# Performance work log

Measured on AMD Instinct MI355X. Metric: run time of the kernel, lower is better.

Reference implementation:

```python
import jax, jax.numpy as jnp
import numpy as np

B, C_IN, S = 2, 512, 1024
D, H, HD = 768, 12, 64
E, K, L = 8, 2, 2
FF = 2048
NFFT, HOP, WIN = 1024, 256, 1024
PAD = (WIN - HOP) // 2
FBINS = NFFT // 2 + 1


def _rope(x):
    # interleaved-pair RoPE over the full hidden dim (module builds RoPE with dim=hidden_dim)
    b, s, d = x.shape
    half = d // 2
    inv = 1.0 / (10000.0 ** (jnp.arange(half, dtype=jnp.float32) / half))
    ang = jnp.arange(s, dtype=jnp.float32)[:, None] * inv[None, :]  # [S, half]
    cos, sin = jnp.cos(ang), jnp.sin(ang)
    xr = x.reshape(b, s, half, 2)
    x1, x2 = xr[..., 0], xr[..., 1]
    return jnp.stack([x1 * cos - x2 * sin, x1 * sin + x2 * cos], -1).reshape(b, s, d)


def _ln(x, g, b):
    m = x.mean(-1, keepdims=True)
    v = ((x - m) ** 2).mean(-1, keepdims=True)
    return (x - m) * jax.lax.rsqrt(v + 1e-5) * g + b


def _attn(x, wq, bq, wk, bk, wv, bv, wo, bo, use_rope):
    b, s, d = x.shape
    q, k, v = x @ wq + bq, x @ wk + bk, x @ wv + bv
    if use_rope:
        q, k = _rope(q), _rope(k)
    q = q.reshape(b, s, H, HD).transpose(0, 2, 1, 3)
    k = k.reshape(b, s, H, HD).transpose(0, 2, 1, 3)
    v = v.reshape(b, s, H, HD).transpose(0, 2, 1, 3)
    scores = jnp.einsum('bhqd,bhkd->bhqk', q, k) * (1.0 / np.sqrt(HD))
    causal = jnp.tril(jnp.ones((s, s), bool))
    scores = jnp.where(causal, scores, jnp.float32(-1e30))
    att = jax.nn.softmax(scores, -1)
    out = jnp.einsum('bhqk,bhkd->bhqd', att, v).transpose(0, 2, 1, 3).reshape(b, s, d)
    return out @ wo + bo


def _moe(x, gw, w1, b1, w2, b2):
    # top-k softmax gating, 2-layer GELU experts, sparse combine
    logits = x @ gw  # [B,S,E]
    topv, topi = jax.lax.top_k(logits, K)
    wts = jax.nn.softmax(topv, -1)  # [B,S,K]
    gate = (wts[..., None] * jax.nn.one_hot(topi, E, dtype=x.dtype)).sum(2)  # [B,S,E]
    h = jax.nn.gelu(jnp.einsum('bsd,edf->bsef', x, w1) + b1)
    y = jnp.einsum('bsef,efd->bsed', h, w2) + b2  # [B,S,E,D]
    return jnp.einsum('bse,bsed->bsd', gate, y)


def _istft_same(spec):
    # Vocos-style 'same' ISTFT: irfft -> window -> overlap-add -> normalize -> trim pad
    b, f, t = spec.shape
    n = jnp.arange(WIN, dtype=jnp.float32)
    win = 0.5 * (1.0 - jnp.cos(2.0 * jnp.pi * n / WIN))  # periodic hann
    frames = jnp.fft.irfft(spec, n=NFFT, axis=1) * win[None, :, None]
    out_len = (t - 1) * HOP + WIN
    idx = ((jnp.arange(t) * HOP)[:, None] + jnp.arange(WIN)[None, :]).reshape(-1)
    y = jnp.zeros((b, out_len), jnp.float32).at[:, idx].add(frames.transpose(0, 2, 1).reshape(b, -1))
    env = jnp.zeros((out_len,), jnp.float32).at[idx].add(jnp.tile(win * win, t))
    return y[:, PAD:-PAD] / env[PAD:-PAD]


def setup_inputs() -> dict:
    key = jax.random.key(0)
    ks = jax.random.split(key, 12)
    r = lambda k, shp: jax.random.normal(k, shp, jnp.float32) * 0.02
    z1 = lambda shp: jnp.zeros(shp, jnp.float32)
    o1 = lambda shp: jnp.ones(shp, jnp.float32)
    return dict(
        z=jax.random.normal(ks[0], (B, C_IN, S), jnp.float32),
        in_w=r(ks[1], (C_IN, D)), in_b=z1((D,)),
        ln1_g=o1((L, D)), ln1_b=z1((L, D)),
        wq=r(ks[2], (L, D, D)), bq=z1((L, D)),
        wk=r(ks[3], (L, D, D)), bk=z1((L, D)),
        wv=r(ks[4], (L, D, D)), bv=z1((L, D)),
        wo=r(ks[5], (L, D, D)), bo=z1((L, D)),
        ln2_g=o1((L, D)), ln2_b=z1((L, D)),
        gate_w=r(ks[6], (L, D, E)),
        e_w1=r(ks[7], (L, E, D, FF)), e_b1=z1((L, E, FF)),
        e_w2=r(ks[8], (L, E, FF, D)), e_b2=z1((L, E, D)),
        out_w=r(ks[9], (D, 2 * FBINS)), out_b=z1((2 * FBINS,)),
    )


def reference(z, in_w, in_b, ln1_g, ln1_b, wq, bq, wk, bk, wv, bv, wo, bo,
              ln2_g, ln2_b, gate_w, e_w1, e_b1, e_w2, e_b2, out_w, out_b):
    # in_projection: ConvTranspose1d with kernel=stride=1 == pointwise linear, then transpose(1,2)
    x = jnp.einsum('bcl,cd->bld', z, in_w) + in_b  # [B,S,D]
    for i in range(L):
        h = _ln(x, ln1_g[i], ln1_b[i])
        x = x + _attn(h, wq[i], bq[i], wk[i], bk[i], wv[i], bv[i], wo[i], bo[i], use_rope=(i == 0))
        h = _ln(x, ln2_g[i], ln2_b[i])
        x = x + _moe(h, gate_w[i], e_w1[i], e_b1[i], e_w2[i], e_b2[i])
    s = x @ out_w + out_b  # [B,S,2*FBINS]
    spec = (s[..., :FBINS] + 1j * s[..., FBINS:]).transpose(0, 2, 1)  # [B,FBINS,T]
    y = _istft_same(spec)
    return y[:, None, :]  # [B,1,OutLen]
```

## Files before the change

### kernel.cpp

```cpp
#include <hip/hip_runtime.h>
#include <hip/hip_bf16.h>
#include <math.h>

#define B_    2
#define CIN   512
#define S_    1024
#define D_    768
#define NH    12
#define HD_   64
#define E_    8
#define FF_   2048
#define T_    2048
#define FBINS 513
#define NS2   1026
#define KPAD  1056
#define NPADO 1152
#define WIN_  1024
#define HOP_  256
#define PAD_  384
#define OUTP  262144
#define AGR   4224

static inline int cdiv(int a, int b) { return (a + b - 1) / b; }

typedef _Float16 half8 __attribute__((ext_vector_type(8)));
typedef __attribute__((ext_vector_type(4))) float floatx4;

#define MFMA16(a, b, c) __builtin_amdgcn_mfma_f32_16x16x32_f16(a, b, c, 0, 0, 0)
#define LO_SCALE 2048.0f
#define LO_INV   (1.0f / 2048.0f)

__device__ inline void split_store(float v, short* p, size_t planeOff) {
    _Float16 h = (_Float16)v;
    _Float16 l = (_Float16)((v - (float)h) * LO_SCALE);
    *(_Float16*)p = h;
    *(_Float16*)(p + planeOff) = l;
}

__device__ inline float gelu_f(float x) {
    float x3 = x * x * x;
    return 0.5f * x * (1.0f + tanhf(0.7978845608028654f * (x + 0.044715f * x3)));
}

__device__ inline void gl_lds16(const short* g, short* l) {
    __builtin_amdgcn_global_load_lds((const __attribute__((address_space(1))) void*)g,
                                     (__attribute__((address_space(3))) void*)l, 16, 0, 0);
}

template <int MODE>
__global__ __launch_bounds__(256) void mm2_k(
    const short* __restrict__ Ah, const short* __restrict__ Al,
    const short* __restrict__ Bh, const short* __restrict__ Bl,
    const float* __restrict__ bias, float* __restrict__ Cf,
    short* __restrict__ Cp, size_t CpPl,
    int Nstore, int K, int SA, int SB, int SC) {
    __shared__ short AsH[2][4096], AsL[2][4096], BsH[2][4096], BsL[2][4096];
    int tid = threadIdx.x;
    int wave = tid >> 6, lane = tid & 63;
    int m0 = blockIdx.y * 128, n0 = blockIdx.x * 128;
    int wm = (wave & 1) * 64, wn = (wave >> 1) * 64;
    floatx4 a1[4][4], a2[4][4];
#pragma unroll
    for (int i = 0; i < 4; ++i)
#pragma unroll
        for (int j = 0; j < 4; ++j) {
            a1[i][j] = (floatx4){0.f, 0.f, 0.f, 0.f};
            a2[i][j] = (floatx4){0.f, 0.f, 0.f, 0.f};
        }
    int lm = lane & 15, lk = (lane >> 4) * 8;
    int fl0 = wave * 64 + lane, fl1 = fl0 + 256;
    int r0 = fl0 >> 2, c0 = (fl0 & 3) * 8;
    int r1 = fl1 >> 2, c1 = (fl1 & 3) * 8;
    int dst0 = wave * 512, dst1 = (wave + 4) * 512;
    int kIters = K >> 5;

    auto stage = [&](int kt, int bb) {
        int k0 = kt << 5;
        size_t a0 = (size_t)(m0 + r0) * SA + k0 + c0;
        size_t a1o = (size_t)(m0 + r1) * SA + k0 + c1;
        size_t b0 = (size_t)(n0 + r0) * SB + k0 + c0;
        size_t b1 = (size_t)(n0 + r1) * SB + k0 + c1;
        gl_lds16(Ah + a0, &AsH[bb][dst0]);
        gl_lds16(Ah + a1o, &AsH[bb][dst1]);
        gl_lds16(Al + a0, &AsL[bb][dst0]);
        gl_lds16(Al + a1o, &AsL[bb][dst1]);
        gl_lds16(Bh + b0, &BsH[bb][dst0]);
        gl_lds16(Bh + b1, &BsH[bb][dst1]);
        gl_lds16(Bl + b0, &BsL[bb][dst0]);
        gl_lds16(Bl + b1, &BsL[bb][dst1]);
    };

    stage(0, 0);
    __syncthreads();
    int cur = 0;
    for (int kt = 0; kt < kIters; ++kt) {
        if (kt + 1 < kIters) stage(kt + 1, cur ^ 1);
        const short* aH = AsH[cur];
        const short* aL = AsL[cur];
        const short* bH = BsH[cur];
        const short* bL = BsL[cur];
        half8 ah[4], al[4], bh[4], bl[4];
#pragma unroll
        for (int i = 0; i < 4; ++i) {
            int off = (wm + i * 16 + lm) * 32 + lk;
            ah[i] = *(const half8*)(aH + off);
            al[i] = *(const half8*)(aL + off);
        }
#pragma unroll
        for (int j = 0; j < 4; ++j) {
            int off = (wn + j * 16 + lm) * 32 + lk;
            bh[j] = *(const half8*)(bH + off);
            bl[j] = *(const half8*)(bL + off);
        }
#pragma unroll
        for (int i = 0; i < 4; ++i)
#pragma unroll
            for (int j = 0; j < 4; ++j) {
                a1[i][j] = MFMA16(ah[i], bh[j], a1[i][j]);
                a2[i][j] = MFMA16(ah[i], bl[j], a2[i][j]);
                a2[i][j] = MFMA16(al[i], bh[j], a2[i][j]);
            }
        __syncthreads();
        cur ^= 1;
    }
    int row4 = (lane >> 4) * 4;
#pragma unroll
    for (int i = 0; i < 4; ++i) {
        int row = m0 + wm + i * 16 + row4;
#pragma unroll
        for (int j = 0; j < 4; ++j) {
            int col = n0 + wn + j * 16 + lm;
            if (col < Nstore) {
                float bv = bias ? bias[col] : 0.0f;
#pragma unroll
                for (int r = 0; r < 4; ++r) {
                    float v = a1[i][j][r] + a2[i][j][r] * LO_INV + bv;
                    size_t idx = (size_t)(row + r) * SC + col;
                    if (MODE == 0) Cf[idx] = v;
                    else if (MODE == 1) Cf[idx] += v;
                    else if (MODE == 2) split_store(v, Cp + idx, CpPl);
                    else split_store(gelu_f(v), Cp + idx, CpPl);
                }
            }
        }
    }
}

template <int MODE>
__global__ __launch_bounds__(256) void mm2_moe_k(
    const short* __restrict__ Agh, const short* __restrict__ Agl,
    const short* __restrict__ BT, size_t eStride, size_t bPl,
    const float* __restrict__ biasAll, int biasStride,
    float* __restrict__ Cf, short* __restrict__ Cp, size_t CpPl,
    const int* __restrict__ counts, const int* __restrict__ offsets,
    int N, int K, int SA, int SB, int SC) {
    int el = blockIdx.z;
    int nrows = counts[el];
    int m0 = blockIdx.y * 128;
    if (m0 >= nrows) return;
    int base = offsets[el];
    const short* Ah = Agh + (size_t)base * SA;
    const short* Al = Agl + (size_t)base * SA;
    const short* Bh = BT + (size_t)el * eStride;
    const short* Bl = Bh + bPl;
    const float* bias = biasAll + (size_t)el * biasStride;
    __shared__ short AsH[2][4096], AsL[2][4096], BsH[2][4096], BsL[2][4096];
    int tid = threadIdx.x;
    int wave = tid >> 6, lane = tid & 63;
    int n0 = blockIdx.x * 128;
    int wm = (wave & 1) * 64, wn = (wave >> 1) * 64;
    floatx4 a1[4][4], a2[4][4];
#pragma unroll
    for (int i = 0; i < 4; ++i)
#pragma unroll
        for (int j = 0; j < 4; ++j) {
            a1[i][j] = (floatx4){0.f, 0.f, 0.f, 0.f};
            a2[i][j] = (floatx4){0.f, 0.f, 0.f, 0.f};
        }
    int lm = lane & 15, lk = (lane >> 4) * 8;
    int fl0 = wave * 64 + lane, fl1 = fl0 + 256;
    int r0 = fl0 >> 2, c0 = (fl0 & 3) * 8;
    int r1 = fl1 >> 2, c1 = (fl1 & 3) * 8;
    int dst0 = wave * 512, dst1 = (wave + 4) * 512;
    int kIters = K >> 5;

    auto stage = [&](int kt, int bb) {
        int k0 = kt << 5;
        size_t a0 = (size_t)(m0 + r0) * SA + k0 + c0;
        size_t a1o = (size_t)(m0 + r1) * SA + k0 + c1;
        size_t b0 = (size_t)(n0 + r0) * SB + k0 + c0;
        size_t b1 = (size_t)(n0 + r1) * SB + k0 + c1;
        gl_lds16(Ah + a0, &AsH[bb][dst0]);
        gl_lds16(Ah + a1o, &AsH[bb][dst1]);
        gl_lds16(Al + a0, &AsL[bb][dst0]);
        gl_lds16(Al + a1o, &AsL[bb][dst1]);
        gl_lds16(Bh + b0, &BsH[bb][dst0]);
        gl_lds16(Bh + b1, &BsH[bb][dst1]);
        gl_lds16(Bl + b0, &BsL[bb][dst0]);
        gl_lds16(Bl + b1, &BsL[bb][dst1]);
    };

    stage(0, 0);
    __syncthreads();
    int cur = 0;
    for (int kt = 0; kt < kIters; ++kt) {
        if (kt + 1 < kIters) stage(kt + 1, cur ^ 1);
        const short* aH = AsH[cur];
        const short* aL = AsL[cur];
        const short* bH = BsH[cur];
        const short* bL = BsL[cur];
        half8 ah[4], al[4], bh[4], bl[4];
#pragma unroll
        for (int i = 0; i < 4; ++i) {
            int off = (wm + i * 16 + lm) * 32 + lk;
            ah[i] = *(const half8*)(aH + off);
            al[i] = *(const half8*)(aL + off);
        }
#pragma unroll
        for (int j = 0; j < 4; ++j) {
            int off = (wn + j * 16 + lm) * 32 + lk;
            bh[j] = *(const half8*)(bH + off);
            bl[j] = *(const half8*)(bL + off);
        }
#pragma unroll
        for (int i = 0; i < 4; ++i)
#pragma unroll
            for (int j = 0; j < 4; ++j) {
                a1[i][j] = MFMA16(ah[i], bh[j], a1[i][j]);
                a2[i][j] = MFMA16(ah[i], bl[j], a2[i][j]);
                a2[i][j] = MFMA16(al[i], bh[j], a2[i][j]);
            }
        __syncthreads();
        cur ^= 1;
    }
    int row4 = (lane >> 4) * 4;
#pragma unroll
    for (int i = 0; i < 4; ++i) {
        int rl = m0 + wm + i * 16 + row4;
#pragma unroll
        for (int j = 0; j < 4; ++j) {
            int col = n0 + wn + j * 16 + lm;
            if (col < N) {
                float bv = bias[col];
#pragma unroll
                for (int r = 0; r < 4; ++r) {
                    if (rl + r < nrows) {
                        float v = a1[i][j][r] + a2[i][j][r] * LO_INV + bv;
                        size_t idx = (size_t)(base + rl + r) * SC + col;
                        if (MODE == 0) Cf[idx] = v;
                        else split_store(gelu_f(v), Cp + idx, CpPl);
                    }
                }
            }
        }
    }
}

__global__ __launch_bounds__(256) void transp2_k(const float* __restrict__ src,
                                                 short* __restrict__ dst, int R, int C, int Cout,
                                                 size_t srcZ, size_t dstZ, size_t planeOff) {
    __shared__ float tile[32][33];
    int z = blockIdx.z;
    src += (size_t)z * srcZ;
    dst += (size_t)z * dstZ;
    int c0 = blockIdx.x * 32, r0 = blockIdx.y * 32;
    int tx = threadIdx.x & 31, ty = threadIdx.x >> 5;
    for (int i = ty; i < 32; i += 8) {
        int r = r0 + i, c = c0 + tx;
        tile[i][tx] = (r < R && c < C) ? src[(size_t)r * C + c] : 0.0f;
    }
    __syncthreads();
    for (int i = ty; i < 32; i += 8) {
        int cc = c0 + i, rr = r0 + tx;
        if (cc < Cout && rr < R) split_store(tile[tx][i], dst + (size_t)cc * R + rr, planeOff);
    }
}

__global__ __launch_bounds__(256) void tz2_k(const float* __restrict__ z, short* __restrict__ xT,
                                             size_t planeOff) {
    int id = blockIdx.x * 256 + threadIdx.x;
    if (id >= T_ * CIN) return;
    int t = id >> 9, c = id & 511;
    int b = t >> 10, l = t & 1023;
    split_store(z[((size_t)b * CIN + c) * S_ + l], xT + id, planeOff);
}

__global__ __launch_bounds__(256) void ln_k(const float* __restrict__ x,
                                            const float* __restrict__ g,
                                            const float* __restrict__ b, short* __restrict__ h,
                                            size_t planeOff) {
    int t = blockIdx.x;
    int tid = threadIdx.x;
    __shared__ float row[D_];
    __shared__ float red[256];
    const float* xr = x + (size_t)t * D_;
    float s = 0.0f;
    for (int i = tid; i < D_; i += 256) {
        float v = xr[i];
        row[i] = v;
        s += v;
    }
    red[tid] = s;
    __syncthreads();
    for (int st = 128; st > 0; st >>= 1) {
        if (tid < st) red[tid] += red[tid + st];
        __syncthreads();
    }
    float mean = red[0] / (float)D_;
    __syncthreads();
    float s2 = 0.0f;
    for (int i = tid; i < D_; i += 256) {
        float d = row[i] - mean;
        s2 += d * d;
    }
    red[tid] = s2;
    __syncthreads();
    for (int st = 128; st > 0; st >>= 1) {
        if (tid < st) red[tid] += red[tid + st];
        __syncthreads();
    }
    float rstd = rsqrtf(red[0] / (float)D_ + 1e-5f);
    for (int i = tid; i < D_; i += 256)
        split_store((row[i] - mean) * rstd * g[i] + b[i], h + (size_t)t * D_ + i, planeOff);
}

__global__ __launch_bounds__(256) void lngate_k(const float* __restrict__ x,
                                                const float* __restrict__ g,
                                                const float* __restrict__ b,
                                                const float* __restrict__ gw,
                                                float* __restrict__ logits) {
    int t = blockIdx.x;
    int tid = threadIdx.x;
    __shared__ float row[D_];
    __shared__ float red[256];
    const float* xr = x + (size_t)t * D_;
    float s = 0.0f;
    for (int i = tid; i < D_; i += 256) {
        float v = xr[i];
        row[i] = v;
        s += v;
    }
    red[tid] = s;
    __syncthreads();
    for (int st = 128; st > 0; st >>= 1) {
        if (tid < st) red[tid] += red[tid + st];
        __syncthreads();
    }
    float mean = red[0] / (float)D_;
    __syncthreads();
    float s2 = 0.0f;
    for (int i = tid; i < D_; i += 256) {
        float d = row[i] - mean;
        s2 += d * d;
    }
    red[tid] = s2;
    __syncthreads();
    for (int st = 128; st > 0; st >>= 1) {
        if (tid < st) red[tid] += red[tid + st];
        __syncthreads();
    }
    float rstd = rsqrtf(red[0] / (float)D_ + 1e-5f);
    __syncthreads();
    int e = tid >> 5, lane = tid & 31;
    float acc = 0.0f;
    for (int d = lane; d < D_; d += 32)
        acc += ((row[d] - mean) * rstd * g[d] + b[d]) * gw[d * E_ + e];
    red[tid] = acc;
    __syncthreads();
    for (int st = 16; st > 0; st >>= 1) {
        if (lane < st) red[tid] += red[tid + st];
        __syncthreads();
    }
    if (lane == 0) logits[t * E_ + e] = red[tid];
}

__global__ void catb_k(const float* __restrict__ a, const float* __restrict__ b,
                       const float* __restrict__ c, float* __restrict__ dst) {
    int i = blockIdx.x * 256 + threadIdx.x;
    if (i < 768) dst[i] = a[i];
    else if (i < 1536) dst[i] = b[i - 768];
    else if (i < 2304) dst[i] = c[i - 1536];
}

__global__ __launch_bounds__(256) void ropesplit_k(const float* __restrict__ qkv,
                                                   short* __restrict__ qd,
                                                   short* __restrict__ kd) {
    int id = blockIdx.x * 256 + threadIdx.x;
    if (id >= T_ * 384) return;
    int t = id / 384, j = id % 384;
    int pos = t & 1023;
    float inv = expf(-(float)j * (9.210340371976184f / 384.0f));
    float ang = (float)pos * inv;
    float sn, cs;
    sincosf(ang, &sn, &cs);
    const float* pq = qkv + (size_t)t * 2304 + 2 * j;
    const float* pk = pq + 768;
    const size_t PL = (size_t)T_ * D_;
    size_t o = (size_t)t * D_ + 2 * j;
    float q1 = pq[0], q2 = pq[1];
    split_store(q1 * cs - q2 * sn, qd + o, PL);
    split_store(q1 * sn + q2 * cs, qd + o + 1, PL);
    float k1 = pk[0], k2 = pk[1];
    split_store(k1 * cs - k2 * sn, kd + o, PL);
    split_store(k1 * sn + k2 * cs, kd + o + 1, PL);
}

__global__ __launch_bounds__(256) void qksplit_k(const float* __restrict__ qkv,
                                                 short* __restrict__ qd,
                                                 short* __restrict__ kd) {
    int id = blockIdx.x * 256 + threadIdx.x;
    if (id >= T_ * D_) return;
    int t = id / D_, c = id % D_;
    const size_t PL = (size_t)T_ * D_;
    split_store(qkv[(size_t)t * 2304 + c], qd + id, PL);
    split_store(qkv[(size_t)t * 2304 + 768 + c], kd + id, PL);
}

__global__ __launch_bounds__(256) void vt2_k(const float* __restrict__ qkv,
                                             short* __restrict__ vp) {
    __shared__ float tile[32][33];
    int bh = blockIdx.z, b = bh / NH, h = bh % NH;
    int j0 = blockIdx.x * 32, d0 = blockIdx.y * 32;
    int tx = threadIdx.x & 31, ty = threadIdx.x >> 5;
    for (int i = ty; i < 32; i += 8)
        tile[i][tx] = qkv[(size_t)(b * S_ + j0 + i) * 2304 + 1536 + h * 64 + d0 + tx];
    __syncthreads();
    for (int i = ty; i < 32; i += 8)
        split_store(tile[tx][i], vp + ((size_t)bh * 64 + d0 + i) * S_ + j0 + tx,
                    (size_t)T_ * D_);
}

__global__ __launch_bounds__(256) void fattn_k(const short* __restrict__ qp,
                                               const short* __restrict__ kp,
                                               const short* __restrict__ vp,
                                               short* __restrict__ ctx) {
    __shared__ short sQ[2][64 * 64];
    __shared__ short sK[2][128 * 64];
    __shared__ short sV[2][64 * 128];
    __shared__ short sP[2][4][16 * 128];
    const size_t PL = (size_t)T_ * D_;
    int qpair = blockIdx.x, bh = blockIdx.y;
    int b = bh / NH, h = bh % NH;
    int tid = threadIdx.x, wave = tid >> 6, lane = tid & 63;
    int quad = lane >> 4, lm = lane & 15;
    int lr8 = lane >> 3;
    int lc8 = ((lane & 7) ^ lr8) * 8;
    int lm7 = lm & 7;

    for (int hh = 0; hh < 2; ++hh) {
        int qt = hh ? (15 - qpair) : qpair;
        int t0 = b * S_ + qt * 64;
        {
#pragma unroll
            for (int pl = 0; pl < 2; ++pl)
#pragma unroll
                for (int c = 0; c < 2; ++c) {
                    int r8 = wave * 16 + c * 8;
                    gl_lds16(qp + pl * PL + (size_t)(t0 + r8 + lr8) * D_ + h * 64 + lc8,
                             &sQ[pl][r8 * 64]);
                }
        }
        floatx4 o1[4], o2[4];
#pragma unroll
        for (int n = 0; n < 4; ++n) {
            o1[n] = (floatx4){0.f, 0.f, 0.f, 0.f};
            o2[n] = (floatx4){0.f, 0.f, 0.f, 0.f};
        }
        float mrow[4] = {-1e30f, -1e30f, -1e30f, -1e30f};
        float lrow[4] = {0.f, 0.f, 0.f, 0.f};
        int ktmax = qt >> 1;
        for (int kt = 0; kt <= ktmax; ++kt) {
            {
#pragma unroll
                for (int pl = 0; pl < 2; ++pl)
#pragma unroll
                    for (int c = 0; c < 4; ++c) {
                        int r8 = wave * 32 + c * 8;
                        gl_lds16(kp + pl * PL +
                                     (size_t)(b * S_ + kt * 128 + r8 + lr8) * D_ + h * 64 + lc8,
                                 &sK[pl][r8 * 64]);
                    }
                int vr = lane >> 4;
#pragma unroll
                for (int pl = 0; pl < 2; ++pl)
#pragma unroll
                    for (int c = 0; c < 4; ++c) {
                        int r4 = wave * 16 + c * 4;
                        int vcs = (((lane & 15) ^ (((c & 1) << 2) + vr))) * 8;
                        gl_lds16(vp + pl * PL + ((size_t)bh * 64 + r4 + vr) * S_ + kt * 128 + vcs,
                                 &sV[pl][r4 * 128]);
                    }
            }
            __syncthreads();
            half8 qh[2], ql[2];
#pragma unroll
            for (int ks = 0; ks < 2; ++ks) {
                int off = (wave * 16 + lm) * 64 + ((ks * 4 + quad) ^ lm7) * 8;
                qh[ks] = *(const half8*)&sQ[0][off];
                ql[ks] = *(const half8*)&sQ[1][off];
            }
            floatx4 sacc[8];
#pragma unroll
            for (int nt = 0; nt < 8; ++nt) {
                floatx4 c1 = (floatx4){0.f, 0.f, 0.f, 0.f};
                floatx4 c2 = (floatx4){0.f, 0.f, 0.f, 0.f};
#pragma unroll
                for (int ks = 0; ks < 2; ++ks) {
                    int off = (nt * 16 + lm) * 64 + ((ks * 4 + quad) ^ lm7) * 8;
                    half8 kh = *(const half8*)&sK[0][off];
                    half8 kl = *(const half8*)&sK[1][off];
                    c1 = MFMA16(qh[ks], kh, c1);
                    c2 = MFMA16(qh[ks], kl, c2);
                    c2 = MFMA16(ql[ks], kh, c2);
                }
#pragma unroll
                for (int r = 0; r < 4; ++r) sacc[nt][r] = (c1[r] + c2[r] * LO_INV) * 0.125f;
            }
            if (kt == ktmax) {
#pragma unroll
                for (int nt = 0; nt < 8; ++nt) {
                    int col = kt * 128 + nt * 16 + lm;
#pragma unroll
                    for (int r = 0; r < 4; ++r) {
                        int rowg = qt * 64 + wave * 16 + quad * 4 + r;
                        if (col > rowg) sacc[nt][r] = -1e30f;
                    }
                }
            }
            float mnew[4], al[4], ls[4];
#pragma unroll
            for (int r = 0; r < 4; ++r) {
                float mx = sacc[0][r];
#pragma unroll
                for (int nt = 1; nt < 8; ++nt) mx = fmaxf(mx, sacc[nt][r]);
#pragma unroll
                for (int msk = 1; msk < 16; msk <<= 1) mx = fmaxf(mx, __shfl_xor(mx, msk));
                mnew[r] = fmaxf(mrow[r], mx);
                al[r] = __expf(mrow[r] - mnew[r]);
                mrow[r] = mnew[r];
                ls[r] = 0.f;
            }
#pragma unroll
            for (int nt = 0; nt < 8; ++nt)
#pragma unroll
                for (int r = 0; r < 4; ++r) {
                    float p = __expf(sacc[nt][r] - mnew[r]);
                    ls[r] += p;
                    _Float16 ph = (_Float16)p;
                    _Float16 plo = (_Float16)((p - (float)ph) * LO_SCALE);
                    int rowp = quad * 4 + r;
                    int off = rowp * 128 + ((nt * 2 + (lm >> 3)) ^ (rowp & 7)) * 8 + (lm & 7);
                    *(_Float16*)&sP[0][wave][off] = ph;
                    *(_Float16*)&sP[1][wave][off] = plo;
                }
#pragma unroll
            for (int r = 0; r < 4; ++r) {
#pragma unroll
                for (int msk = 1; msk < 16; msk <<= 1) ls[r] += __shfl_xor(ls[r], msk);
                lrow[r] = lrow[r] * al[r] + ls[r];
            }
#pragma unroll
            for (int n = 0; n < 4; ++n)
#pragma unroll
                for (int r = 0; r < 4; ++r) {
                    o1[n][r] *= al[r];
                    o2[n][r] *= al[r];
                }
            half8 ph8[4], pl8[4];
#pragma unroll
            for (int ks = 0; ks < 4; ++ks) {
                int off = lm * 128 + ((ks * 4 + quad) ^ lm7) * 8;
                ph8[ks] = *(const half8*)&sP[0][wave][off];
                pl8[ks] = *(const half8*)&sP[1][wave][off];
            }
#pragma unroll
            for (int nt2 = 0; nt2 < 4; ++nt2) {
#pragma unroll
                for (int ks = 0; ks < 4; ++ks) {
                    int off = (nt2 * 16 + lm) * 128 + ((ks * 4 + quad) ^ lm7) * 8;
                    half8 vh = *(const half8*)&sV[0][off];
                    half8 vl = *(const half8*)&sV[1][off];
                    o1[nt2] = MFMA16(ph8[ks], vh, o1[nt2]);
                    o2[nt2] = MFMA16(ph8[ks], vl, o2[nt2]);
                    o2[nt2] = MFMA16(pl8[ks], vh, o2[nt2]);
                }
            }
            __syncthreads();
        }
#pragma unroll
        for (int r = 0; r < 4; ++r) {
            float inv = 1.0f / lrow[r];
            int rowg = t0 + wave * 16 + quad * 4 + r;
#pragma unroll
            for (int nt2 = 0; nt2 < 4; ++nt2) {
                float val = (o1[nt2][r] + o2[nt2][r] * LO_INV) * inv;
                int col = h * 64 + nt2 * 16 + lm;
                split_store(val, ctx + (size_t)rowg * D_ + col, PL);
            }
        }
    }
}

__global__ void zero_meta_k(int* __restrict__ counts) {
    int i = threadIdx.x;
    if (i < E_) counts[i] = 0;
}

__global__ __launch_bounds__(256) void top2_k(const float* __restrict__ logits,
                                              int* __restrict__ counts, int* __restrict__ tokE,
                                              float* __restrict__ tokW) {
    int t = blockIdx.x * 256 + threadIdx.x;
    if (t >= T_) return;
    const float* l = logits + t * E_;
    int i0 = 0;
    float v0 = l[0];
    for (int e = 1; e < E_; ++e) {
        float v = l[e];
        if (v > v0) { v0 = v; i0 = e; }
    }
    int i1 = -1;
    float v1 = -1e30f;
    for (int e = 0; e < E_; ++e) {
        if (e == i0) continue;
        float v = l[e];
        if (v > v1) { v1 = v; i1 = e; }
    }
    float e2 = expf(v1 - v0);
    float w0 = 1.0f / (1.0f + e2);
    float w1 = e2 * w0;
    tokE[2 * t] = i0;
    tokE[2 * t + 1] = i1;
    tokW[2 * t] = w0;
    tokW[2 * t + 1] = w1;
    atomicAdd(&counts[i0], 1);
    atomicAdd(&counts[i1], 1);
}

__global__ void offsets_k(const int* __restrict__ counts, int* __restrict__ offsets,
                          int* __restrict__ cursor) {
    if (threadIdx.x == 0 && blockIdx.x == 0) {
        int a = 0;
        for (int e = 0; e < E_; ++e) {
            offsets[e] = a;
            cursor[e] = a;
            a += counts[e];
        }
    }
}

__global__ __launch_bounds__(256) void assign_k(const int* __restrict__ tokE,
                                                int* __restrict__ cursor,
                                                int* __restrict__ rowTok,
                                                int* __restrict__ tokRow) {
    int t = blockIdx.x * 256 + threadIdx.x;
    if (t >= T_) return;
    for (int s = 0; s < 2; ++s) {
        int e = tokE[2 * t + s];
        int r = atomicAdd(&cursor[e], 1);
        rowTok[r] = t;
        tokRow[2 * t + s] = r;
    }
}

__global__ __launch_bounds__(256) void gather2_k(const short* __restrict__ h,
                                                 const int* __restrict__ rowTok,
                                                 short* __restrict__ Ag, size_t hPl, size_t aPl) {
    int id = blockIdx.x * 256 + threadIdx.x;
    if (id >= 2 * T_ * 96) return;
    int p = blockIdx.y;
    int r = id / 96, c = id % 96;
    const uint4* src = (const uint4*)(h + p * hPl) + (size_t)rowTok[r] * 96 + c;
    ((uint4*)(Ag + p * aPl))[(size_t)r * 96 + c] = *src;
}

__global__ __launch_bounds__(256) void combine_k(const float* __restrict__ y2,
                                                 const int* __restrict__ tokRow,
                                                 const float* __restrict__ tokW,
                                                 float* __restrict__ x, short* __restrict__ xb,
                                                 size_t xbPl) {
    int id = blockIdx.x * 256 + threadIdx.x;
    if (id >= T_ * D_) return;
    int t = id / D_;
    float v = x[id] + tokW[2 * t] * y2[(size_t)tokRow[2 * t] * D_ + id % D_] +
              tokW[2 * t + 1] * y2[(size_t)tokRow[2 * t + 1] * D_ + id % D_];
    x[id] = v;
    split_store(v, xb + id, xbPl);
}

__global__ void pad_outb_k(const float* __restrict__ outb, float* __restrict__ obp) {
    int i = blockIdx.x * 256 + threadIdx.x;
    if (i < NPADO) obp[i] = (i < NS2) ? outb[i] : 0.0f;
}

__global__ __launch_bounds__(256) void basisT2_k(short* __restrict__ bT, size_t planeOff) {
    int id = blockIdx.x * 256 + threadIdx.x;
    if (id >= WIN_ * KPAD) return;
    int n = id / KPAD, j = id % KPAD;
    float val = 0.0f;
    if (j < NS2) {
        float wn = 0.5f - 0.5f * cosf(6.283185307179586f * (float)n / 1024.0f);
        int kf = (j < FBINS) ? j : (j - FBINS);
        float scale = (kf == 0 || kf == 512) ? (1.0f / 1024.0f) : (2.0f / 1024.0f);
        int m = (kf * n) & 1023;
        float th = 6.283185307179586f * (float)m / 1024.0f;
        if (j < FBINS) val = scale * cosf(th);
        else val = (kf == 0 || kf == 512) ? 0.0f : (-scale * sinf(th));
        val *= wn;
    }
    split_store(val, bT + id, planeOff);
}

__global__ __launch_bounds__(256) void ola_k(const float* __restrict__ frames,
                                             float* __restrict__ out, int total) {
    int id = blockIdx.x * 256 + threadIdx.x;
    if (id >= total) return;
    int b = id / OUTP, pout = id % OUTP;
    int p = pout + PAD_;
    int t1 = p >> 8;
    if (t1 > S_ - 1) t1 = S_ - 1;
    int t0 = p - (WIN_ - 1) + (HOP_ - 1);
    t0 = (t0 > 0) ? (t0 >> 8) : 0;
    float acc = 0.0f, env = 0.0f;
    for (int t = t0; t <= t1; ++t) {
        int n = p - (t << 8);
        float wn = 0.5f - 0.5f * cosf(6.283185307179586f * (float)n / 1024.0f);
        acc += frames[(((size_t)(b * S_ + t)) << 10) + n];
        env += wn * wn;
    }
    out[id] = acc / env;
}

extern "C" void kernel_launch(void* const* d_in, const int* in_sizes, int n_in, void* d_out,
                              int out_size, void* d_ws, size_t ws_size, hipStream_t stream) {
    const float* z    = (const float*)d_in[0];
    const float* in_w = (const float*)d_in[1];
    const float* in_b = (const float*)d_in[2];
    const float* ln1g = (const float*)d_in[3];
    const float* ln1b = (const float*)d_in[4];
    const float* wq   = (const float*)d_in[5];
    const float* bq   = (const float*)d_in[6];
    const float* wk   = (const float*)d_in[7];
    const float* bk   = (const float*)d_in[8];
    const float* wv   = (const float*)d_in[9];
    const float* bv   = (const float*)d_in[10];
    const float* wo   = (const float*)d_in[11];
    const float* bo   = (const float*)d_in[12];
    const float* ln2g = (const float*)d_in[13];
    const float* ln2b = (const float*)d_in[14];
    const float* gw   = (const float*)d_in[15];
    const float* ew1  = (const float*)d_in[16];
    const float* eb1  = (const float*)d_in[17];
    const float* ew2  = (const float*)d_in[18];
    const float* eb2  = (const float*)d_in[19];
    const float* outw = (const float*)d_in[20];
    const float* outb = (const float*)d_in[21];

    float* ws = (float*)d_ws;
    int* wsi = (int*)d_ws;
    const size_t TD = (size_t)T_ * D_;
    const size_t o_x      = 0;
    const size_t o_logits = TD;
    const size_t o_counts = o_logits + (size_t)T_ * E_;
    const size_t o_cursor = o_counts + 16;
    const size_t o_offs   = o_cursor + 16;
    const size_t o_tokE   = o_offs + 16;
    const size_t o_rowTok = o_tokE + 2 * T_;
    const size_t o_tokRow = o_rowTok + 2 * T_;
    const size_t o_tokW   = o_tokRow + 2 * T_;
    const size_t o_obp    = o_tokW + 2 * T_;
    const size_t o_W      = ((o_obp + NPADO + 127) / 128) * 128;
    const size_t WSLOT    = (size_t)D_ * D_;
    const size_t o_q      = o_W + 4 * WSLOT;
    const size_t o_k      = o_q + TD;
    const size_t o_v      = o_k + TD;
    const size_t o_h      = o_v + TD;
    const size_t o_ctx    = o_h + TD;
    const size_t o_eT     = o_ctx + TD;
    const size_t o_Ag     = o_eT + 2 * (size_t)FF_ * D_;
    const size_t AgF      = (size_t)AGR * D_;
    const size_t total    = o_Ag + AgF;
    if (ws_size < total * sizeof(float)) return;
    const size_t o_h1     = o_W;
    const size_t o_y2     = o_Ag;
    const size_t o_zT     = o_eT;
    const size_t o_s      = o_eT;
    const size_t o_basisT = o_s + (size_t)T_ * KPAD;
    const size_t o_frames = o_basisT + (size_t)WIN_ * KPAD;
    const size_t o_qp     = o_eT;
    const size_t o_kp     = o_eT + TD;
    const size_t o_vp     = o_eT + 2 * TD;
    const size_t PL_TD   = TD;
    const size_t PL_W    = (size_t)D_ * D_;
    const size_t PL_INW  = (size_t)D_ * CIN;
    const size_t PL_OUTW = (size_t)NPADO * D_;
    const size_t PL_E    = (size_t)FF_ * D_;
    const size_t EST     = 2 * PL_E;
    const size_t PL_AG   = (size_t)AGR * D_;
    const size_t PL_H1   = (size_t)AGR * FF_;
    const size_t PL_ZT   = (size_t)T_ * CIN;
    const size_t PL_S    = (size_t)T_ * KPAD;
    const size_t PL_BAS  = (size_t)WIN_ * KPAD;

    dim3 blk(256);
    short* Wsh  = (short*)(ws + o_W);
    short* hP   = (short*)(ws + o_h);
    short* ctxP = (short*)(ws + o_ctx);
    short* eTP  = (short*)(ws + o_eT);
    short* AgP  = (short*)(ws + o_Ag);
    short* h1P  = (short*)(ws + o_h1);
    short* qpP  = (short*)(ws + o_qp);
    short* kpP  = (short*)(ws + o_kp);
    short* vpP  = (short*)(ws + o_vp);

    tz2_k<<<cdiv(T_ * CIN, 256), blk, 0, stream>>>(z, (short*)(ws + o_zT), PL_ZT);
    transp2_k<<<dim3(24, 16, 1), blk, 0, stream>>>(in_w, Wsh, CIN, D_, D_, 0, 0, PL_INW);
    mm2_k<0><<<dim3(6, 16), blk, 0, stream>>>((short*)(ws + o_zT), (short*)(ws + o_zT) + PL_ZT,
                                              Wsh, Wsh + PL_INW, in_b, ws + o_x, nullptr, 0,
                                              D_, CIN, CIN, CIN, D_);

    for (int i = 0; i < 2; ++i) {
        const size_t wOff = (size_t)i * D_ * D_;
        const size_t bOff = (size_t)i * D_;
        transp2_k<<<dim3(24, 24, 1), blk, 0, stream>>>(wq + wOff, Wsh, D_, D_, D_, 0, 0, 3 * PL_W);
        transp2_k<<<dim3(24, 24, 1), blk, 0, stream>>>(wk + wOff, Wsh + PL_W, D_, D_, D_, 0, 0, 3 * PL_W);
        transp2_k<<<dim3(24, 24, 1), blk, 0, stream>>>(wv + wOff, Wsh + 2 * PL_W, D_, D_, D_, 0, 0, 3 * PL_W);
        transp2_k<<<dim3(24, 24, 1), blk, 0, stream>>>(wo + wOff, Wsh + 6 * PL_W, D_, D_, D_, 0, 0, PL_W);
        catb_k<<<cdiv(2304, 256), blk, 0, stream>>>(bq + bOff, bk + bOff, bv + bOff,
                                                    ws + o_logits);

        ln_k<<<T_, blk, 0, stream>>>(ws + o_x, ln1g + bOff, ln1b + bOff, hP, PL_TD);
        mm2_k<0><<<dim3(18, 16), blk, 0, stream>>>(hP, hP + PL_TD, Wsh, Wsh + 3 * PL_W,
                                                   ws + o_logits, ws + o_q, nullptr, 0,
                                                   2304, D_, D_, D_, 2304);
        if (i == 0) {
            ropesplit_k<<<cdiv(T_ * 384, 256), blk, 0, stream>>>(ws + o_q, qpP, kpP);
        } else {
            qksplit_k<<<cdiv(T_ * D_, 256), blk, 0, stream>>>(ws + o_q, qpP, kpP);
        }
        vt2_k<<<dim3(32, 2, B_ * NH), blk, 0, stream>>>(ws + o_q, vpP);
        fattn_k<<<dim3(8, B_ * NH), blk, 0, stream>>>(qpP, kpP, vpP, ctxP);
        mm2_k<1><<<dim3(6, 16), blk, 0, stream>>>(ctxP, ctxP + PL_TD, Wsh + 6 * PL_W,
                                                  Wsh + 7 * PL_W, bo + bOff, ws + o_x,
                                                  nullptr, 0, D_, D_, D_, D_, D_);
        ln_k<<<T_, blk, 0, stream>>>(ws + o_x, ln2g + bOff, ln2b + bOff, hP, PL_TD);
        lngate_k<<<T_, blk, 0, stream>>>(ws + o_x, ln2g + bOff, ln2b + bOff,
                                         gw + (size_t)i * D_ * E_, ws + o_logits);
        zero_meta_k<<<1, 64, 0, stream>>>(wsi + o_counts);
        top2_k<<<cdiv(T_, 256), blk, 0, stream>>>(ws + o_logits, wsi + o_counts, wsi + o_tokE,
                                                  ws + o_tokW);
        offsets_k<<<1, 64, 0, stream>>>(wsi + o_counts, wsi + o_offs, wsi + o_cursor);
        assign_k<<<cdiv(T_, 256), blk, 0, stream>>>(wsi + o_tokE, wsi + o_cursor, wsi + o_rowTok,
                                                    wsi + o_tokRow);
        gather2_k<<<dim3(cdiv(2 * T_ * 96, 256), 2), blk, 0, stream>>>(hP, wsi + o_rowTok, AgP,
                                                                       PL_TD, PL_AG);
        for (int g = 0; g < 4; ++g) {
            transp2_k<<<dim3(64, 24, 2), blk, 0, stream>>>(
                ew1 + ((size_t)i * E_ + 2 * g) * D_ * FF_, eTP, D_, FF_, FF_,
                (size_t)D_ * FF_, EST, PL_E);
            mm2_moe_k<3><<<dim3(16, 33, 2), blk, 0, stream>>>(
                AgP, AgP + PL_AG, eTP, EST, PL_E, eb1 + (size_t)i * E_ * FF_ + 2 * g * FF_, FF_,
                nullptr, h1P, PL_H1, wsi + o_counts + 2 * g, wsi + o_offs + 2 * g,
                FF_, D_, D_, D_, FF_);
        }
        for (int g = 0; g < 4; ++g) {
            transp2_k<<<dim3(24, 64, 2), blk, 0, stream>>>(
                ew2 + ((size_t)i * E_ + 2 * g) * FF_ * D_, eTP, FF_, D_, D_,
                (size_t)FF_ * D_, EST, PL_E);
            mm2_moe_k<0><<<dim3(6, 33, 2), blk, 0, stream>>>(
                h1P, h1P + PL_H1, eTP, EST, PL_E, eb2 + (size_t)i * E_ * D_ + 2 * g * D_, D_,
                ws + o_y2, nullptr, 0, wsi + o_counts + 2 * g, wsi + o_offs + 2 * g,
                D_, FF_, FF_, FF_, D_);
        }
        combine_k<<<cdiv(T_ * D_, 256), blk, 0, stream>>>(ws + o_y2, wsi + o_tokRow, ws + o_tokW,
                                                          ws + o_x, ctxP, PL_TD);
    }

    transp2_k<<<dim3(36, 24, 1), blk, 0, stream>>>(outw, Wsh, D_, NS2, NPADO, 0, 0, PL_OUTW);
    pad_outb_k<<<cdiv(NPADO, 256), blk, 0, stream>>>(outb, ws + o_obp);
    mm2_k<2><<<dim3(NPADO / 128, 16), blk, 0, stream>>>(ctxP, ctxP + PL_TD, Wsh, Wsh + PL_OUTW,
                                                        ws + o_obp, nullptr, (short*)(ws + o_s),
                                                        PL_S, KPAD, D_, D_, D_, KPAD);
    basisT2_k<<<cdiv(WIN_ * KPAD, 256), blk, 0, stream>>>((short*)(ws + o_basisT), PL_BAS);
    mm2_k<0><<<dim3(8, 16), blk, 0, stream>>>((short*)(ws + o_s), (short*)(ws + o_s) + PL_S,
                                              (short*)(ws + o_basisT),
                                              (short*)(ws + o_basisT) + PL_BAS, nullptr,
                                              ws + o_frames, nullptr, 0, WIN_, KPAD, KPAD, KPAD,
                                              WIN_);
    ola_k<<<cdiv(out_size, 256), blk, 0, stream>>>(ws + o_frames, (float*)d_out, out_size);
}
```

Before: 2.134 ms.

## Add split-K with atomic accumulation to under-filled GEMMs

Adds a split-K mode to the dense and MoE split-fp16 GEMM kernels. Each block handles a slice of the K loop and accumulates its result into a zero-initialized fp32 output with atomicAdd, and only the first slice adds the bias. This is applied to the input projection, the attention output projection, the second MoE expert GEMM and the ISTFT basis GEMM, which previously launched too few blocks (96–128) to fill the GPU. In exchange it adds zero-fill kernels, atomic traffic and a summation order that is no longer deterministic.

```diff
diff --git a/kernel.cpp b/kernel.cpp
--- a/kernel.cpp
+++ b/kernel.cpp
@@ -47,6 +47,11 @@
                                      (__attribute__((address_space(3))) void*)l, 16, 0, 0);
 }
 
+__global__ __launch_bounds__(256) void zerof_k(float* __restrict__ p, int n4) {
+    int i = blockIdx.x * 256 + threadIdx.x;
+    if (i < n4) ((float4*)p)[i] = make_float4(0.f, 0.f, 0.f, 0.f);
+}
+
 template <int MODE>
 __global__ __launch_bounds__(256) void mm2_k(
     const short* __restrict__ Ah, const short* __restrict__ Al,
@@ -58,6 +63,10 @@
     int tid = threadIdx.x;
     int wave = tid >> 6, lane = tid & 63;
     int m0 = blockIdx.y * 128, n0 = blockIdx.x * 128;
+    int kcz = blockIdx.z;
+    int kIters = K >> 5;
+    int kcIters = kIters / (int)gridDim.z;
+    int ktBase = kcz * kcIters, ktEnd = ktBase + kcIters;
     int wm = (wave & 1) * 64, wn = (wave >> 1) * 64;
     floatx4 a1[4][4], a2[4][4];
 #pragma unroll
@@ -72,7 +81,6 @@
     int r0 = fl0 >> 2, c0 = (fl0 & 3) * 8;
     int r1 = fl1 >> 2, c1 = (fl1 & 3) * 8;
     int dst0 = wave * 512, dst1 = (wave + 4) * 512;
-    int kIters = K >> 5;
 
     auto stage = [&](int kt, int bb) {
         int k0 = kt << 5;
@@ -90,11 +98,11 @@
         gl_lds16(Bl + b1, &BsL[bb][dst1]);
     };
 
-    stage(0, 0);
+    stage(ktBase, 0);
     __syncthreads();
     int cur = 0;
-    for (int kt = 0; kt < kIters; ++kt) {
-        if (kt + 1 < kIters) stage(kt + 1, cur ^ 1);
+    for (int kt = ktBase; kt < ktEnd; ++kt) {
+        if (kt + 1 < ktEnd) stage(kt + 1, cur ^ 1);
         const short* aH = AsH[cur];
         const short* aL = AsL[cur];
         const short* bH = BsH[cur];
@@ -132,12 +140,13 @@
             int col = n0 + wn + j * 16 + lm;
             if (col < Nstore) {
                 float bv = bias ? bias[col] : 0.0f;
+                if (MODE == 1 && kcz != 0) bv = 0.0f;
 #pragma unroll
                 for (int r = 0; r < 4; ++r) {
                     float v = a1[i][j][r] + a2[i][j][r] * LO_INV + bv;
                     size_t idx = (size_t)(row + r) * SC + col;
                     if (MODE == 0) Cf[idx] = v;
-                    else if (MODE == 1) Cf[idx] += v;
+                    else if (MODE == 1) atomicAdd(&Cf[idx], v);
                     else if (MODE == 2) split_store(v, Cp + idx, CpPl);
                     else split_store(gelu_f(v), Cp + idx, CpPl);
                 }
@@ -146,7 +155,7 @@
     }
 }
 
-template <int MODE>
+template <int MODE, int KS>
 __global__ __launch_bounds__(256) void mm2_moe_k(
     const short* __restrict__ Agh, const short* __restrict__ Agl,
     const short* __restrict__ BT, size_t eStride, size_t bPl,
@@ -156,7 +165,8 @@
     int N, int K, int SA, int SB, int SC) {
     int el = blockIdx.z;
     int nrows = counts[el];
-    int m0 = blockIdx.y * 128;
+    int kc = blockIdx.y & ((1 << KS) - 1);
+    int m0 = (blockIdx.y >> KS) * 128;
     if (m0 >= nrows) return;
     int base = offsets[el];
     const short* Ah = Agh + (size_t)base * SA;
@@ -169,6 +179,9 @@
     int wave = tid >> 6, lane = tid & 63;
     int n0 = blockIdx.x * 128;
     int wm = (wave & 1) * 64, wn = (wave >> 1) * 64;
+    int kIters = K >> 5;
+    int kcIters = kIters >> KS;
+    int ktBase = kc * kcIters, ktEnd = ktBase + kcIters;
     floatx4 a1[4][4], a2[4][4];
 #pragma unroll
     for (int i = 0; i < 4; ++i)
@@ -182,7 +195,6 @@
     int r0 = fl0 >> 2, c0 = (fl0 & 3) * 8;
     int r1 = fl1 >> 2, c1 = (fl1 & 3) * 8;
     int dst0 = wave * 512, dst1 = (wave + 4) * 512;
-    int kIters = K >> 5;
 
     auto stage = [&](int kt, int bb) {
         int k0 = kt << 5;
@@ -200,11 +212,11 @@
         gl_lds16(Bl + b1, &BsL[bb][dst1]);
     };
 
-    stage(0, 0);
+    stage(ktBase, 0);
     __syncthreads();
     int cur = 0;
-    for (int kt = 0; kt < kIters; ++kt) {
-        if (kt + 1 < kIters) stage(kt + 1, cur ^ 1);
+    for (int kt = ktBase; kt < ktEnd; ++kt) {
+        if (kt + 1 < ktEnd) stage(kt + 1, cur ^ 1);
         const short* aH = AsH[cur];
         const short* aL = AsL[cur];
         const short* bH = BsH[cur];
@@ -242,12 +254,13 @@
             int col = n0 + wn + j * 16 + lm;
             if (col < N) {
                 float bv = bias[col];
+                if (MODE == 0 && kc != 0) bv = 0.0f;
 #pragma unroll
                 for (int r = 0; r < 4; ++r) {
                     if (rl + r < nrows) {
                         float v = a1[i][j][r] + a2[i][j][r] * LO_INV + bv;
                         size_t idx = (size_t)(base + rl + r) * SC + col;
-                        if (MODE == 0) Cf[idx] = v;
+                        if (MODE == 0) atomicAdd(&Cf[idx], v);
                         else split_store(gelu_f(v), Cp + idx, CpPl);
                     }
                 }
@@ -814,9 +827,10 @@
 
     tz2_k<<<cdiv(T_ * CIN, 256), blk, 0, stream>>>(z, (short*)(ws + o_zT), PL_ZT);
     transp2_k<<<dim3(24, 16, 1), blk, 0, stream>>>(in_w, Wsh, CIN, D_, D_, 0, 0, PL_INW);
-    mm2_k<0><<<dim3(6, 16), blk, 0, stream>>>((short*)(ws + o_zT), (short*)(ws + o_zT) + PL_ZT,
-                                              Wsh, Wsh + PL_INW, in_b, ws + o_x, nullptr, 0,
-                                              D_, CIN, CIN, CIN, D_);
+    zerof_k<<<cdiv((int)(TD / 4), 256), blk, 0, stream>>>(ws + o_x, (int)(TD / 4));
+    mm2_k<1><<<dim3(6, 16, 2), blk, 0, stream>>>((short*)(ws + o_zT), (short*)(ws + o_zT) + PL_ZT,
+                                                 Wsh, Wsh + PL_INW, in_b, ws + o_x, nullptr, 0,
+                                                 D_, CIN, CIN, CIN, D_);
 
     for (int i = 0; i < 2; ++i) {
         const size_t wOff = (size_t)i * D_ * D_;
@@ -839,9 +853,9 @@
         }
         vt2_k<<<dim3(32, 2, B_ * NH), blk, 0, stream>>>(ws + o_q, vpP);
         fattn_k<<<dim3(8, B_ * NH), blk, 0, stream>>>(qpP, kpP, vpP, ctxP);
-        mm2_k<1><<<dim3(6, 16), blk, 0, stream>>>(ctxP, ctxP + PL_TD, Wsh + 6 * PL_W,
-                                                  Wsh + 7 * PL_W, bo + bOff, ws + o_x,
-                                                  nullptr, 0, D_, D_, D_, D_, D_);
+        mm2_k<1><<<dim3(6, 16, 4), blk, 0, stream>>>(ctxP, ctxP + PL_TD, Wsh + 6 * PL_W,
+                                                     Wsh + 7 * PL_W, bo + bOff, ws + o_x,
+                                                     nullptr, 0, D_, D_, D_, D_, D_);
         ln_k<<<T_, blk, 0, stream>>>(ws + o_x, ln2g + bOff, ln2b + bOff, hP, PL_TD);
         lngate_k<<<T_, blk, 0, stream>>>(ws + o_x, ln2g + bOff, ln2b + bOff,
                                          gw + (size_t)i * D_ * E_, ws + o_logits);
@@ -857,16 +871,17 @@
             transp2_k<<<dim3(64, 24, 2), blk, 0, stream>>>(
                 ew1 + ((size_t)i * E_ + 2 * g) * D_ * FF_, eTP, D_, FF_, FF_,
                 (size_t)D_ * FF_, EST, PL_E);
-            mm2_moe_k<3><<<dim3(16, 33, 2), blk, 0, stream>>>(
+            mm2_moe_k<3, 0><<<dim3(16, 33, 2), blk, 0, stream>>>(
                 AgP, AgP + PL_AG, eTP, EST, PL_E, eb1 + (size_t)i * E_ * FF_ + 2 * g * FF_, FF_,
                 nullptr, h1P, PL_H1, wsi + o_counts + 2 * g, wsi + o_offs + 2 * g,
                 FF_, D_, D_, D_, FF_);
         }
+        zerof_k<<<cdiv(4096 * D_ / 4, 256), blk, 0, stream>>>(ws + o_y2, 4096 * D_ / 4);
         for (int g = 0; g < 4; ++g) {
             transp2_k<<<dim3(24, 64, 2), blk, 0, stream>>>(
                 ew2 + ((size_t)i * E_ + 2 * g) * FF_ * D_, eTP, FF_, D_, D_,
                 (size_t)FF_ * D_, EST, PL_E);
-            mm2_moe_k<0><<<dim3(6, 33, 2), blk, 0, stream>>>(
+            mm2_moe_k<0, 2><<<dim3(6, 132, 2), blk, 0, stream>>>(
                 h1P, h1P + PL_H1, eTP, EST, PL_E, eb2 + (size_t)i * E_ * D_ + 2 * g * D_, D_,
                 ws + o_y2, nullptr, 0, wsi + o_counts + 2 * g, wsi + o_offs + 2 * g,
                 D_, FF_, FF_, FF_, D_);
@@ -881,10 +896,12 @@
                                                         ws + o_obp, nullptr, (short*)(ws + o_s),
                                                         PL_S, KPAD, D_, D_, D_, KPAD);
     basisT2_k<<<cdiv(WIN_ * KPAD, 256), blk, 0, stream>>>((short*)(ws + o_basisT), PL_BAS);
-    mm2_k<0><<<dim3(8, 16), blk, 0, stream>>>((short*)(ws + o_s), (short*)(ws + o_s) + PL_S,
-                                              (short*)(ws + o_basisT),
-                                              (short*)(ws + o_basisT) + PL_BAS, nullptr,
-                                              ws + o_frames, nullptr, 0, WIN_, KPAD, KPAD, KPAD,
-                                              WIN_);
+    zerof_k<<<cdiv((int)(B_ * S_ * WIN_ / 4), 256), blk, 0, stream>>>(ws + o_frames,
+                                                                      B_ * S_ * WIN_ / 4);
+    mm2_k<1><<<dim3(8, 16, 3), blk, 0, stream>>>((short*)(ws + o_s), (short*)(ws + o_s) + PL_S,
+                                                 (short*)(ws + o_basisT),
+                                                 (short*)(ws + o_basisT) + PL_BAS, nullptr,
+                                                 ws + o_frames, nullptr, 0, WIN_, KPAD, KPAD, KPAD,
+                                                 WIN_);
     ola_k<<<cdiv(out_size, 256), blk, 0, stream>>>(ws + o_frames, (float*)d_out, out_size);
 }
```

New measurement: 1.772 ms. -17.0%, faster.
